# Performance work log

Hardware: AMD Instinct MI355X
Metric: run time of the kernel (lower is better)

## Reference

```python
import jax, jax.numpy as jnp
import numpy as np

QN = 5.0  # params['mich']['Q_n']
# lb/ub for ['R_1','1/R_1C_1','OCV - U','-M_H','K_H','x','y'] (mich)
LB = jnp.array([0.0, 0.0, 0.05, 0.0, 0.0, 0.04236, 0.023], dtype=jnp.float32)
UB = jnp.array([0.04, 1e-06, 0.8, 0.0, 0.0, 0.84, 0.84804], dtype=jnp.float32)


def ocv_curve_mich(ocv_params):
    x = ocv_params[..., 0:1]
    y = ocv_params[..., 1:2]
    Up = (4.4167 - 1.6518 * y + 1.6225 * y**2 - 2.0843 * y**3 + 3.5146 * y**4
          - 2.2166 * y**5 - 4 * jnp.exp(109.451 * y - 100.006))
    Un = (0.063 + 0.8 * jnp.exp(-75 * (x + 0.001))
          - 0.012 * jnp.tanh((x - 0.127) / 0.016)
          - 0.0118 * jnp.tanh((x - 0.155) / 0.016)
          - 0.0035 * jnp.tanh((x - 0.22) / 0.02)
          - 0.0095 * jnp.tanh((x - 0.19) / 0.013)
          - 0.0145 * jnp.tanh((x - 0.49) / 0.02)
          - 0.08 * jnp.tanh((x - 1.03) / 0.055))
    return Up - Un


def setup_inputs() -> dict:
    key = jax.random.key(0)
    kX, kSC, k1, k2, k3, k4 = jax.random.split(key, 6)
    B, T = 512, 8192
    X = jax.random.normal(kX, (B, T, 3), dtype=jnp.float32)
    SC = jax.random.normal(kSC, (B, 2), dtype=jnp.float32)
    W1 = jax.random.normal(k1, (3, 6), dtype=jnp.float32) * 0.5
    b1 = jax.random.normal(k2, (6,), dtype=jnp.float32) * 0.1
    W2 = jax.random.normal(k3, (6, 7), dtype=jnp.float32) * 0.5
    b2 = jax.random.normal(k4, (7,), dtype=jnp.float32) * 0.1
    return {"X": X, "SC": SC, "W1": W1, "b1": b1, "W2": W2, "b2": b2}


def reference(X, SC, W1, b1, W2, b2):
    t = X[..., 0:1]      # [B,T,1]
    I = X[..., 1:2]      # [B,T,1]
    Temp = X[..., 2:3]   # [B,T,1]
    Q = SC[..., 0:1]     # [B,1]
    R0 = SC[..., 1:2]    # [B,1]

    # Coulomb-counting SOC (trapezoidal), cumulative over time
    dSOC = (I[:, 1:, :] + I[:, :-1, :]) * (t[:, 1:, :] - t[:, :-1, :]) / (2.0 * 3600.0 * QN)
    SOC = jnp.cumsum(jnp.concatenate([jnp.zeros_like(I[:, :1, :]), dSOC], axis=1), axis=1)
    SOC = SOC + Q[:, None, :] / QN  # [B,T,1]

    Tmean = jnp.nanmean(Temp, axis=1, keepdims=True)  # [B,1,1]
    x = jnp.concatenate([SOC,
                         jnp.broadcast_to(R0[:, None, :], SOC.shape),
                         jnp.broadcast_to(Tmean, SOC.shape)], axis=-1)  # [B,T,3]

    h = jax.nn.softplus(x @ W1 + b1)
    p = h @ W2 + b2
    theta = LB + (UB - LB) * jax.nn.sigmoid(0.01 * p)  # [B,T,7]

    R1 = theta[..., 0:1]
    R1C1r = theta[..., 1:2]
    OCV_U = theta[..., 2:3]
    mMH = theta[..., 3:4]
    KH = theta[..., 4:5]
    OCV = ocv_curve_mich(theta[..., 5:])  # [B,T,1]

    # Faithful quirk of source: odeint's t_mask selects channel 0 of
    # X_ode = [I, R_1, 1/R_1C_1, -M_H, K_H], so dt_i = I_{i+1} - I_i.
    dt = I[:, 1:, 0] - I[:, :-1, 0]  # [B, T-1]

    UH0 = jnp.zeros_like(Q)                         # [B,1]
    U10 = -OCV_U[:, 0, :] - UH0 - I[:, 0, :] * R0   # [B,1]
    y0 = jnp.concatenate([UH0, U10], axis=-1)       # [B,2]

    def step(y, inp):
        dti, Ii, R1i, Ci, Mi, Ki = inp
        UH = y[:, 0:1]
        U1 = y[:, 1:2]
        dUH = -Ki * Ii * (-Mi - UH)
        dU1 = Ci * (R1i * Ii - U1)
        ynew = y + dti[:, None] * jnp.concatenate([dUH, dU1], axis=-1)
        return ynew, ynew

    # Euler integration uses params at step i (not i+1): slice [:, :-1, :]
    xs = (dt.T,
          I[:, :-1, :].transpose(1, 0, 2),
          R1[:, :-1, :].transpose(1, 0, 2),
          R1C1r[:, :-1, :].transpose(1, 0, 2),
          mMH[:, :-1, :].transpose(1, 0, 2),
          KH[:, :-1, :].transpose(1, 0, 2))
    _, ys = jax.lax.scan(step, y0, xs)              # ys: [T-1,B,2]
    voltages = jnp.concatenate([y0[None], ys], axis=0).transpose(1, 0, 2)  # [B,T,2]

    UH = voltages[..., 0:1]
    U1 = voltages[..., 1:2]
    pred_U = OCV + UH + U1 + I * R0[:, None, :]     # [B,T,1]
    return pred_U
```

## Files before the change

kernel.cpp:

```cpp
#include <hip/hip_runtime.h>
#include <math.h>


#define TT    8192
#define BLK   512
#define NW    8
#define EPT   16
#define NNODE 128
#define PADJ(j) ((j) + ((j) >> 5))

__device__ __forceinline__ float frcp(float x) { return __builtin_amdgcn_rcpf(x); }
__device__ __forceinline__ float fsig(float x) { return frcp(1.0f + __expf(-x)); }
__device__ __forceinline__ float ftanh_x(float x) {
    return 1.0f - 2.0f * frcp(__expf(2.0f * x) + 1.0f);
}
__device__ __forceinline__ float fsoftplus_x(float z) {
    return fmaxf(z, 0.0f) + __logf(1.0f + __expf(-fabsf(z)));
}

__device__ __forceinline__ void eval_chain(float soc,
    const float* __restrict__ w1, const float* __restrict__ pre1,
    const float* __restrict__ w2, const float* __restrict__ bb2,
    float& OCV, float& R1, float& C, float& OCVU)
{
    float h[6];
    #pragma unroll
    for (int i = 0; i < 6; ++i)
        h[i] = fsoftplus_x(fmaf(soc, w1[i], pre1[i]));
    float p0 = bb2[0], p1 = bb2[1], p2 = bb2[2], p5 = bb2[5], p6 = bb2[6];
    #pragma unroll
    for (int i = 0; i < 6; ++i) {
        p0 = fmaf(h[i], w2[7*i + 0], p0);
        p1 = fmaf(h[i], w2[7*i + 1], p1);
        p2 = fmaf(h[i], w2[7*i + 2], p2);
        p5 = fmaf(h[i], w2[7*i + 5], p5);
        p6 = fmaf(h[i], w2[7*i + 6], p6);
    }
    R1   = 0.04f * fsig(0.01f * p0);
    C    = 1e-6f * fsig(0.01f * p1);
    OCVU = fmaf(0.75f,    fsig(0.01f * p2), 0.05f);
    float ox = fmaf(0.79764f, fsig(0.01f * p5), 0.04236f);
    float oy = fmaf(0.82504f, fsig(0.01f * p6), 0.023f);
    float up = fmaf(oy, fmaf(oy, fmaf(oy, fmaf(oy, fmaf(oy, -2.2166f, 3.5146f),
                    -2.0843f), 1.6225f), -1.6518f), 4.4167f);
    up -= 4.0f * __expf(fmaf(109.451f, oy, -100.006f));
    float un = 0.063f + 0.8f * __expf(-75.0f * (ox + 0.001f));
    un = fmaf(-0.012f,  ftanh_x((ox - 0.127f) * 62.5f),        un);
    un = fmaf(-0.0118f, ftanh_x((ox - 0.155f) * 62.5f),        un);
    un = fmaf(-0.0035f, ftanh_x((ox - 0.22f)  * 50.0f),        un);
    un = fmaf(-0.0095f, ftanh_x((ox - 0.19f)  * 76.9230769f),  un);
    un = fmaf(-0.0145f, ftanh_x((ox - 0.49f)  * 50.0f),        un);
    un = fmaf(-0.08f,   ftanh_x((ox - 1.03f)  * 18.1818182f),  un);
    OCV = up - un;
}

__global__ void __launch_bounds__(BLK, 4)
voltnet_kernel(const float* __restrict__ X, const float* __restrict__ SC,
               const float* __restrict__ W1, const float* __restrict__ b1,
               const float* __restrict__ W2, const float* __restrict__ b2,
               float* __restrict__ out)
{
    __shared__ float  ldsT[PADJ(TT - 1) + 2];
    __shared__ float  ldsI[PADJ(TT - 1) + 2];
    __shared__ float  tw[NW], dw[NW], mnw[NW], mxw[NW], sA[NW], sB[NW];
    __shared__ float4 nodes[NNODE];
    __shared__ float  U1arr[BLK];
    __shared__ float  bcU10;

    const int b    = blockIdx.x;
    const int tid  = threadIdx.x;
    const int lane = tid & 63;
    const int wv   = tid >> 6;
    const int s    = tid * EPT;

    const float* __restrict__ Xrow = X + (size_t)b * TT * 3;
    const float Q  = SC[2 * b + 0];
    const float R0 = SC[2 * b + 1];

    float w1[18], bb1[6], w2[42], bb2[7];
    #pragma unroll
    for (int i = 0; i < 18; ++i) w1[i] = W1[i];
    #pragma unroll
    for (int i = 0; i < 6;  ++i) bb1[i] = b1[i];
    #pragma unroll
    for (int i = 0; i < 42; ++i) w2[i] = W2[i];
    #pragma unroll
    for (int i = 0; i < 7;  ++i) bb2[i] = b2[i];

    float tsum = 0.0f;
    #pragma unroll 4
    for (int it = 0; it < EPT; ++it) {
        int j = tid + it * BLK;
        float tt = Xrow[3 * j + 0];
        float ii = Xrow[3 * j + 1];
        float tp = Xrow[3 * j + 2];
        ldsT[PADJ(j)] = tt;
        ldsI[PADJ(j)] = ii;
        tsum += tp;
    }
    #pragma unroll
    for (int d = 32; d > 0; d >>= 1) tsum += __shfl_down(tsum, d, 64);
    if (lane == 0) tw[wv] = tsum;
    __syncthreads();

    float Tsum = 0.0f;
    #pragma unroll
    for (int w = 0; w < NW; ++w) Tsum += tw[w];
    const float Tmean = Tsum * (1.0f / (float)TT);

    float pre1[6];
    #pragma unroll
    for (int o = 0; o < 6; ++o)
        pre1[o] = fmaf(R0, w1[6 + o], fmaf(Tmean, w1[12 + o], bb1[o]));

    float tprev = 0.0f, iprev = 0.0f;
    if (tid > 0) { tprev = ldsT[PADJ(s - 1)]; iprev = ldsI[PADJ(s - 1)]; }
    const float inext_last = (tid < BLK - 1) ? ldsI[PADJ(s + EPT)] : 0.0f;
    __syncthreads();

    float lp = 0.0f;
    float mnl = 1e30f, mxl = -1e30f;
    #pragma unroll 4
    for (int e = 0; e < EPT; ++e) {
        int j = s + e;
        float tt = ldsT[PADJ(j)];
        float ii = ldsI[PADJ(j)];
        float ds = (ii + iprev) * (tt - tprev) * (1.0f / 36000.0f);
        if (j == 0) ds = 0.0f;
        lp += ds;
        ldsT[PADJ(j)] = lp;
        mnl = fminf(mnl, lp);
        mxl = fmaxf(mxl, lp);
        tprev = tt; iprev = ii;
    }
    float inc = lp;
    #pragma unroll
    for (int d = 1; d < 64; d <<= 1) {
        float v = __shfl_up(inc, d, 64);
        if (lane >= d) inc += v;
    }
    if (lane == 63) dw[wv] = inc;
    __syncthreads();
    float woff = 0.0f;
    for (int w = 0; w < wv; ++w) woff += dw[w];
    const float soc_base = fmaf(Q, 0.2f, woff + (inc - lp));

    float mn_t = soc_base + mnl, mx_t = soc_base + mxl;
    #pragma unroll
    for (int d = 32; d > 0; d >>= 1) {
        mn_t = fminf(mn_t, __shfl_down(mn_t, d, 64));
        mx_t = fmaxf(mx_t, __shfl_down(mx_t, d, 64));
    }
    if (lane == 0) { mnw[wv] = mn_t; mxw[wv] = mx_t; }
    __syncthreads();
    float lo = 1e30f, hi = -1e30f;
    #pragma unroll
    for (int w = 0; w < NW; ++w) { lo = fminf(lo, mnw[w]); hi = fmaxf(hi, mxw[w]); }
    {
        float pad = fmaf(hi - lo, 1.0f / 256.0f, 1e-7f);
        lo -= pad; hi += pad;
    }
    const float hstep = (hi - lo) * (1.0f / (float)(NNODE - 1));
    const float invh  = (float)(NNODE - 1) * frcp(hi - lo);

    if (tid < NNODE) {
        float OCV, R1v, Cv, OCVU;
        eval_chain(fmaf((float)tid, hstep, lo), w1, pre1, w2, bb2, OCV, R1v, Cv, OCVU);
        nodes[tid] = make_float4(OCV, R1v, Cv, 0.0f);
    }
    if (tid == 0) {
        float OCV, R1v, Cv, OCVU;
        eval_chain(soc_base, w1, pre1, w2, bb2, OCV, R1v, Cv, OCVU);
        bcU10 = -OCVU - ldsI[PADJ(0)] * R0;
    }
    __syncthreads();

    float Ap = 1.0f, Bp = 0.0f;
    #pragma unroll 4
    for (int e = 0; e < EPT; ++e) {
        int j = s + e;
        float soc = soc_base + ldsT[PADJ(j)];
        float ii  = ldsI[PADJ(j)];
        float inx = (e == EPT - 1) ? inext_last : ldsI[PADJ(j + 1)];

        float u  = (soc - lo) * invh;
        int   k  = (int)u;
        k = (k < 0) ? 0 : ((k > NNODE - 2) ? NNODE - 2 : k);
        float fr = u - (float)k;
        float4 n0 = nodes[k];
        float4 n1 = nodes[k + 1];
        float OCV = fmaf(fr, n1.x - n0.x, n0.x);
        float R1v = fmaf(fr, n1.y - n0.y, n0.y);
        float Cv  = fmaf(fr, n1.z - n0.z, n0.z);

        ldsT[PADJ(j)] = fmaf(ii, R0, OCV) + Bp;
        ldsI[PADJ(j)] = Ap;

        float g  = (inx - ii) * Cv;
        float aj = 1.0f - g;
        float bj = g * R1v * ii;
        if (j == TT - 1) { aj = 1.0f; bj = 0.0f; }
        Bp = fmaf(aj, Bp, bj);
        Ap = aj * Ap;
    }

    float A = Ap, B = Bp;
    #pragma unroll
    for (int d = 1; d < 64; d <<= 1) {
        float Au = __shfl_up(A, d, 64);
        float Bu = __shfl_up(B, d, 64);
        if (lane >= d) { B = fmaf(A, Bu, B); A = A * Au; }
    }
    float Aex = __shfl_up(A, 1, 64);
    float Bex = __shfl_up(B, 1, 64);
    if (lane == 0) { Aex = 1.0f; Bex = 0.0f; }
    if (lane == 63) { sA[wv] = A; sB[wv] = B; }
    __syncthreads();
    float Ao = 1.0f, Bo = 0.0f;
    for (int w = 0; w < wv; ++w) {
        Bo = fmaf(sA[w], Bo, sB[w]);
        Ao = sA[w] * Ao;
    }
    const float U1s = fmaf(Aex * Ao, bcU10, fmaf(Aex, Bo, Bex));
    U1arr[tid] = U1s;
    __syncthreads();

    float* __restrict__ orow = out + (size_t)b * TT;
    #pragma unroll 4
    for (int it = 0; it < EPT; ++it) {
        int j = tid + it * BLK;
        float v = fmaf(ldsI[PADJ(j)], U1arr[j >> 4], ldsT[PADJ(j)]);
        __builtin_nontemporal_store(v, &orow[j]);
    }
}

extern "C" void kernel_launch(void* const* d_in, const int* in_sizes, int n_in,
                              void* d_out, int out_size, void* d_ws, size_t ws_size,
                              hipStream_t stream)
{
    const float* X  = (const float*)d_in[0];
    const float* SC = (const float*)d_in[1];
    const float* W1 = (const float*)d_in[2];
    const float* b1 = (const float*)d_in[3];
    const float* W2 = (const float*)d_in[4];
    const float* b2 = (const float*)d_in[5];
    float* outp = (float*)d_out;
    const int B = in_sizes[1] / 2;
    hipLaunchKernelGGL(voltnet_kernel, dim3(B), dim3(BLK), 0, stream,
                       X, SC, W1, b1, W2, b2, outp);
}
```

Measured before the change: 104.2 us.

## Keep per-thread scan intermediates in registers and store output as float4

Each thread's cumulative SOC values and currents now stay in register arrays across the three phases instead of being written back to and reread from LDS. The min/max range reduction is merged with the prefix-sum exchange, which removes two block barriers. The final output is written directly from registers as contiguous float4 nontemporal stores of each thread's 16 elements, dropping the U1arr staging buffer and its barrier. This raises register pressure by 32 floats per thread, which could reduce occupancy under launch_bounds(512,4), and the stores are no longer coalesced across lanes at element stride.

```diff
diff --git a/kernel.cpp b/kernel.cpp
--- a/kernel.cpp
+++ b/kernel.cpp
@@ -8,6 +8,8 @@
 #define EPT   16
 #define NNODE 128
 #define PADJ(j) ((j) + ((j) >> 5))
+
+typedef float vfloat4 __attribute__((ext_vector_type(4)));
 
 __device__ __forceinline__ float frcp(float x) { return __builtin_amdgcn_rcpf(x); }
 __device__ __forceinline__ float fsig(float x) { return frcp(1.0f + __expf(-x)); }
@@ -64,7 +66,6 @@
     __shared__ float  ldsI[PADJ(TT - 1) + 2];
     __shared__ float  tw[NW], dw[NW], mnw[NW], mxw[NW], sA[NW], sB[NW];
     __shared__ float4 nodes[NNODE];
-    __shared__ float  U1arr[BLK];
     __shared__ float  bcU10;
 
     const int b    = blockIdx.x;
@@ -116,9 +117,9 @@
     float tprev = 0.0f, iprev = 0.0f;
     if (tid > 0) { tprev = ldsT[PADJ(s - 1)]; iprev = ldsI[PADJ(s - 1)]; }
     const float inext_last = (tid < BLK - 1) ? ldsI[PADJ(s + EPT)] : 0.0f;
-    __syncthreads();
-
-    float lp = 0.0f;
+
+    float lp[EPT], Ireg[EPT];
+    float run = 0.0f;
     float mnl = 1e30f, mxl = -1e30f;
     #pragma unroll 4
     for (int e = 0; e < EPT; ++e) {
@@ -127,36 +128,44 @@
         float ii = ldsI[PADJ(j)];
         float ds = (ii + iprev) * (tt - tprev) * (1.0f / 36000.0f);
         if (j == 0) ds = 0.0f;
-        lp += ds;
-        ldsT[PADJ(j)] = lp;
-        mnl = fminf(mnl, lp);
-        mxl = fmaxf(mxl, lp);
+        run += ds;
+        lp[e]   = run;
+        Ireg[e] = ii;
+        mnl = fminf(mnl, run);
+        mxl = fmaxf(mxl, run);
         tprev = tt; iprev = ii;
     }
-    float inc = lp;
+    float inc = run;
     #pragma unroll
     for (int d = 1; d < 64; d <<= 1) {
         float v = __shfl_up(inc, d, 64);
         if (lane >= d) inc += v;
     }
-    if (lane == 63) dw[wv] = inc;
-    __syncthreads();
-    float woff = 0.0f;
-    for (int w = 0; w < wv; ++w) woff += dw[w];
-    const float soc_base = fmaf(Q, 0.2f, woff + (inc - lp));
-
-    float mn_t = soc_base + mnl, mx_t = soc_base + mxl;
+    float mn_t = (inc - run) + mnl, mx_t = (inc - run) + mxl;
     #pragma unroll
     for (int d = 32; d > 0; d >>= 1) {
         mn_t = fminf(mn_t, __shfl_down(mn_t, d, 64));
         mx_t = fmaxf(mx_t, __shfl_down(mx_t, d, 64));
     }
+    if (lane == 63) dw[wv] = inc;
     if (lane == 0) { mnw[wv] = mn_t; mxw[wv] = mx_t; }
     __syncthreads();
+
+    float woff = 0.0f;
+    for (int w = 0; w < wv; ++w) woff += dw[w];
+    const float soc_base = fmaf(Q, 0.2f, woff + (inc - run));
+
     float lo = 1e30f, hi = -1e30f;
-    #pragma unroll
-    for (int w = 0; w < NW; ++w) { lo = fminf(lo, mnw[w]); hi = fmaxf(hi, mxw[w]); }
     {
+        float acc = 0.0f;
+        #pragma unroll
+        for (int w = 0; w < NW; ++w) {
+            lo = fminf(lo, acc + mnw[w]);
+            hi = fmaxf(hi, acc + mxw[w]);
+            acc += dw[w];
+        }
+        lo = fmaf(Q, 0.2f, lo);
+        hi = fmaf(Q, 0.2f, hi);
         float pad = fmaf(hi - lo, 1.0f / 256.0f, 1e-7f);
         lo -= pad; hi += pad;
     }
@@ -170,18 +179,17 @@
     }
     if (tid == 0) {
         float OCV, R1v, Cv, OCVU;
-        eval_chain(soc_base, w1, pre1, w2, bb2, OCV, R1v, Cv, OCVU);
-        bcU10 = -OCVU - ldsI[PADJ(0)] * R0;
+        eval_chain(Q * 0.2f, w1, pre1, w2, bb2, OCV, R1v, Cv, OCVU);
+        bcU10 = -OCVU - Ireg[0] * R0;
     }
     __syncthreads();
 
     float Ap = 1.0f, Bp = 0.0f;
     #pragma unroll 4
     for (int e = 0; e < EPT; ++e) {
-        int j = s + e;
-        float soc = soc_base + ldsT[PADJ(j)];
-        float ii  = ldsI[PADJ(j)];
-        float inx = (e == EPT - 1) ? inext_last : ldsI[PADJ(j + 1)];
+        float soc = soc_base + lp[e];
+        float ii  = Ireg[e];
+        float inx = (e == EPT - 1) ? inext_last : Ireg[e + 1];
 
         float u  = (soc - lo) * invh;
         int   k  = (int)u;
@@ -193,13 +201,13 @@
         float R1v = fmaf(fr, n1.y - n0.y, n0.y);
         float Cv  = fmaf(fr, n1.z - n0.z, n0.z);
 
-        ldsT[PADJ(j)] = fmaf(ii, R0, OCV) + Bp;
-        ldsI[PADJ(j)] = Ap;
+        lp[e]   = fmaf(ii, R0, OCV) + Bp;
+        Ireg[e] = Ap;
 
         float g  = (inx - ii) * Cv;
         float aj = 1.0f - g;
         float bj = g * R1v * ii;
-        if (j == TT - 1) { aj = 1.0f; bj = 0.0f; }
+        if (s + e == TT - 1) { aj = 1.0f; bj = 0.0f; }
         Bp = fmaf(aj, Bp, bj);
         Ap = aj * Ap;
     }
@@ -222,15 +230,16 @@
         Ao = sA[w] * Ao;
     }
     const float U1s = fmaf(Aex * Ao, bcU10, fmaf(Aex, Bo, Bex));
-    U1arr[tid] = U1s;
-    __syncthreads();
-
-    float* __restrict__ orow = out + (size_t)b * TT;
-    #pragma unroll 4
-    for (int it = 0; it < EPT; ++it) {
-        int j = tid + it * BLK;
-        float v = fmaf(ldsI[PADJ(j)], U1arr[j >> 4], ldsT[PADJ(j)]);
-        __builtin_nontemporal_store(v, &orow[j]);
+
+    float* __restrict__ obase = out + (size_t)b * TT + s;
+    #pragma unroll
+    for (int c = 0; c < 4; ++c) {
+        vfloat4 o;
+        o.x = fmaf(Ireg[4 * c + 0], U1s, lp[4 * c + 0]);
+        o.y = fmaf(Ireg[4 * c + 1], U1s, lp[4 * c + 1]);
+        o.z = fmaf(Ireg[4 * c + 2], U1s, lp[4 * c + 2]);
+        o.w = fmaf(Ireg[4 * c + 3], U1s, lp[4 * c + 3]);
+        __builtin_nontemporal_store(o, (vfloat4*)(obase + 4 * c));
     }
 }
 
```

Result: slower. 114.7 us (+10.0%).
